# Performance work log

Hardware: AMD Instinct MI355X
Metric: run time of the kernel (lower is better)

The kernel has to match this reference:

```python
import jax, jax.numpy as jnp
import numpy as np

L = 5   # local window size (l)
R = 2   # upsample factor (r)


def setup_inputs() -> dict:
    key = jax.random.key(0)
    k0, k1, k2 = jax.random.split(key, 3)
    B, C, H, W, OUT = 4, 128, 64, 64, 128
    x = jax.random.normal(k0, (B, C, H, W), jnp.float32)
    # conv1: in_channels -> l^2, 3x3, pad 1 (with bias, as nn.Conv2d default)
    w1 = jax.random.normal(k1, (L * L, C, 3, 3), jnp.float32) * 0.05
    b1 = jnp.zeros((L * L,), jnp.float32)
    # conv2: 4*in_channels -> out_channels, 1x1 (stored as [out, 4C])
    w2 = jax.random.normal(k2, (OUT, 4 * C), jnp.float32) * 0.05
    b2 = jnp.zeros((OUT,), jnp.float32)
    return {"x": x, "w1": w1, "b1": b1, "w2": w2, "b2": b2}


def _upsample2_nearest(t):
    # nearest-neighbor x2 upsample on NCHW
    return jnp.repeat(jnp.repeat(t, R, axis=2), R, axis=3)


def reference(x, w1, b1, w2, b2):
    B, C, H, W = x.shape
    # conv1 (3x3, SAME) -> [B, L^2, H, W]
    k = jax.lax.conv_general_dilated(
        x, w1, window_strides=(1, 1), padding='SAME',
        dimension_numbers=('NCHW', 'OIHW', 'NCHW')) + b1[None, :, None, None]
    # nearest x2 upsample then softmax over the L^2 channel dim
    k = _upsample2_nearest(k)                 # [B, L^2, 2H, 2W]
    k = jax.nn.softmax(k, axis=1)
    # non-overlapping RxR block extraction (unfold size=R, step=R twice)
    # -> [B, L^2, H, W, R^2], last-dim order (row-offset, col-offset)
    k = k.reshape(B, L * L, H, R, W, R).transpose(0, 1, 2, 4, 3, 5)
    k = k.reshape(B, L * L, H, W, R * R)
    # overlapping LxL window extraction of the input (unfold size=L, step=1)
    pad = L // 2
    xp = jnp.pad(x, ((0, 0), (0, 0), (pad, pad), (pad, pad)))
    wins = jnp.stack(
        [xp[:, :, i:i + H, j:j + W] for i in range(L) for j in range(L)],
        axis=-1)                               # [B, C, H, W, L^2]
    # per-pixel matmul: [C, L^2] @ [L^2, R^2] -> [B, H, W, C, R^2]
    out = jnp.einsum('bchwk,bkhwr->bhwcr', wins, k)
    # flatten (C, R^2) -> 4C (C-major, matching torch reshape), back to NCHW
    out = out.reshape(B, H, W, C * R * R).transpose(0, 3, 1, 2)
    out = _upsample2_nearest(out)              # [B, 4C, 2H, 2W]
    # conv2: 1x1 -> out_channels
    out = jnp.einsum('bchw,oc->bohw', out, w2) + b2[None, :, None, None]
    return out
```

## Files before the change

### kernel.cpp

```cpp
#include <hip/hip_runtime.h>
#include <math.h>

#define BB   4
#define CC   128
#define HH   64
#define WW   64
#define OUTC 128
#define KK   25

typedef __attribute__((ext_vector_type(8))) short short8;
typedef __attribute__((ext_vector_type(4))) float floatx4;

__device__ __forceinline__ unsigned short f32_to_bf16(float v) {
    unsigned int u = __float_as_uint(v);
    u += 0x7fffu + ((u >> 16) & 1u);
    return (unsigned short)(u >> 16);
}
__device__ __forceinline__ float bf16_to_f32(unsigned short h) {
    return __uint_as_float(((unsigned int)h) << 16);
}

__global__ void prep_kernel(const float* __restrict__ w2,
                            const float* __restrict__ w1,
                            unsigned short* __restrict__ w2o,
                            unsigned short* __restrict__ w1f) {
    int i = blockIdx.x * 256 + threadIdx.x;
    if (i < 16384) {
        int o = i >> 7, c = i & 127;
        const float* p = w2 + o * (4 * CC) + c * 4;
        w2o[o * CC + c] = f32_to_bf16(p[0] + p[1] + p[2] + p[3]);
    } else {
        int f = i - 16384;
        int i8 = f & 7;  int rest = f >> 3;
        int lane = rest & 63; rest >>= 6;
        int ks = rest & 3;  rest >>= 2;
        int mt = rest & 1;  rest >>= 1;
        int dydx = rest % 9;
        int wt   = rest / 9;
        int kk = mt * 16 + (lane & 15);
        int c  = ks * 32 + (lane >> 4) * 8 + i8;
        unsigned short o16 = 0;
        if (kk < KK) {
            float v = w1[(size_t)(kk * CC + c) * 9 + dydx];
            unsigned short hi = f32_to_bf16(v);
            o16 = wt ? f32_to_bf16(v - bf16_to_f32(hi)) : hi;
        }
        w1f[f] = o16;
    }
}

__global__ __launch_bounds__(512, 2) void fused_kernel(
        const float* __restrict__ x,
        const unsigned short* __restrict__ w1f,
        const unsigned short* __restrict__ w2o,
        const float* __restrict__ b1,
        const float* __restrict__ b2,
        float* __restrict__ out) {
    __shared__ unsigned short xs_hi[3 * 68 * 128];
    __shared__ unsigned short xs_lo[3 * 68 * 128];
    __shared__ float pk[KK * 64];
    __shared__ float blds[32];
    unsigned short* sKT = xs_hi;

    int bid0 = blockIdx.x;
    int bid  = (bid0 & 7) * 32 + (bid0 >> 3);
    int h = bid & 63;
    int b = bid >> 6;
    int t = threadIdx.x;
    int lane = t & 63;
    int wv = t >> 6;

    const float* xb = x + (size_t)b * CC * (HH * WW);

    if (t < KK) blds[t] = b1[t];
    {
        int j = lane + 2;
        int swz = (j & 15) << 3;
        for (int ci = 0; ci < 16; ++ci) {
            int c  = wv * 16 + ci;
            int cs = c ^ swz;
            const float* xc = xb + (size_t)c * (HH * WW);
            #pragma unroll
            for (int r = 0; r < 3; ++r) {
                int y = h - 1 + r;
                float v = (y >= 0 && y < HH) ? xc[y * WW + lane] : 0.f;
                unsigned short hi = f32_to_bf16(v);
                unsigned short lo = f32_to_bf16(v - bf16_to_f32(hi));
                xs_hi[(r * 68 + j) * 128 + cs] = hi;
                xs_lo[(r * 68 + j) * 128 + cs] = lo;
            }
        }
        for (int i = t; i < 3 * 4 * 128; i += 512) {
            int c = i & 127; int rem = i >> 7;
            int jj = rem & 3; int r = rem >> 2;
            int j2 = (jj < 2) ? jj : 64 + jj;
            int cs2 = c ^ ((j2 & 15) << 3);
            xs_hi[(r * 68 + j2) * 128 + cs2] = 0;
            xs_lo[(r * 68 + j2) * 128 + cs2] = 0;
        }
    }
    __syncthreads();

    int fpx = lane & 15, quad = lane >> 4;
    int mt = wv & 1, ntw = wv >> 1;
    int pxb = ntw * 16 + fpx;
    floatx4 acc = {0.f, 0.f, 0.f, 0.f};
    for (int dydx = 0; dydx < 9; ++dydx) {
        int r   = dydx / 3;
        int dxm = dydx - 3 * r;
        int j   = pxb + dxm + 1;
        int rowbase = (r * 68 + j) * 128;
        int swz = (j & 15) << 3;
        const unsigned short* whb = w1f + (dydx * 2 + mt) * 2048 + lane * 8;
        #pragma unroll
        for (int ks = 0; ks < 4; ++ks) {
            int cb = (ks * 32 + quad * 8) ^ swz;
            short8 Ah = *(const short8*)(whb + ks * 512);
            short8 Al = *(const short8*)(whb + 36864 + ks * 512);
            short8 Bh = *(const short8*)&xs_hi[rowbase + cb];
            short8 Bl = *(const short8*)&xs_lo[rowbase + cb];
            acc = __builtin_amdgcn_mfma_f32_16x16x32_bf16(Ah, Bh, acc, 0, 0, 0);
            acc = __builtin_amdgcn_mfma_f32_16x16x32_bf16(Ah, Bl, acc, 0, 0, 0);
            acc = __builtin_amdgcn_mfma_f32_16x16x32_bf16(Al, Bh, acc, 0, 0, 0);
        }
    }
    #pragma unroll
    for (int reg = 0; reg < 4; ++reg) {
        int kk = mt * 16 + quad * 4 + reg;
        if (kk < KK) pk[kk * 64 + pxb] = acc[reg] + blds[kk];
    }
    __syncthreads();

    int pp2 = t & 31, cw = t >> 5;

    float2 lg[KK];
    #pragma unroll
    for (int k = 0; k < KK; ++k) lg[k] = *(const float2*)&pk[k * 64 + 2 * pp2];
    float m0 = -1e30f, m1 = -1e30f;
    #pragma unroll
    for (int k = 0; k < KK; ++k) { m0 = fmaxf(m0, lg[k].x); m1 = fmaxf(m1, lg[k].y); }
    float s0 = 0.f, s1 = 0.f;
    #pragma unroll
    for (int k = 0; k < KK; ++k) {
        lg[k].x = __expf(lg[k].x - m0); s0 += lg[k].x;
        lg[k].y = __expf(lg[k].y - m1); s1 += lg[k].y;
    }
    float i0 = 1.f / s0, i1 = 1.f / s1;
    #pragma unroll
    for (int k = 0; k < KK; ++k) { lg[k].x *= i0; lg[k].y *= i1; }

    int colg = 2 * pp2 - 2;
    int coff[3]; float cmask[3];
    #pragma unroll
    for (int jx = 0; jx < 3; ++jx) {
        int cg = colg + 2 * jx;
        cmask[jx] = (cg >= 0 && cg <= WW - 2) ? 1.f : 0.f;
        coff[jx]  = min(max(cg, 0), WW - 2);
    }
    int yoff[5]; float msk[15];
    #pragma unroll
    for (int di = 0; di < 5; ++di) {
        int y = h + di - 2;
        float rm = (y >= 0 && y < HH) ? 1.f : 0.f;
        yoff[di] = min(max(y, 0), HH - 1) * WW;
        #pragma unroll
        for (int jx = 0; jx < 3; ++jx) msk[di * 3 + jx] = rm * cmask[jx];
    }

    #pragma unroll 2
    for (int i8 = 0; i8 < 8; ++i8) {
        int c = i8 * 16 + cw;
        const float* xc = xb + (size_t)c * (HH * WW);
        float2 xv[15];
        #pragma unroll
        for (int di = 0; di < 5; ++di)
            #pragma unroll
            for (int jx = 0; jx < 3; ++jx) {
                float2 v = *(const float2*)(xc + yoff[di] + coff[jx]);
                float mm = msk[di * 3 + jx];
                xv[di * 3 + jx] = make_float2(v.x * mm, v.y * mm);
            }
        float t0 = 0.f, t1 = 0.f;
        #pragma unroll
        for (int di = 0; di < 5; ++di) {
            float2 x01 = xv[di * 3 + 0];
            float2 x23 = xv[di * 3 + 1];
            float2 x45 = xv[di * 3 + 2];
            t0 += lg[di*5+0].x * x01.x + lg[di*5+1].x * x01.y
                + lg[di*5+2].x * x23.x + lg[di*5+3].x * x23.y
                + lg[di*5+4].x * x45.x;
            t1 += lg[di*5+0].y * x01.y + lg[di*5+1].y * x23.x
                + lg[di*5+2].y * x23.y + lg[di*5+3].y * x45.x
                + lg[di*5+4].y * x45.y;
        }
        sKT[(2 * pp2) * 136 + c]     = f32_to_bf16(t0);
        sKT[(2 * pp2 + 1) * 136 + c] = f32_to_bf16(t1);
    }
    __syncthreads();

    floatx4 am[4] = {{0.f,0.f,0.f,0.f},{0.f,0.f,0.f,0.f},
                     {0.f,0.f,0.f,0.f},{0.f,0.f,0.f,0.f}};
    #pragma unroll
    for (int ks = 0; ks < 4; ++ks) {
        short8 af = *(const short8*)&w2o[(size_t)(16*wv + fpx) * CC + ks*32 + quad*8];
        #pragma unroll
        for (int nt = 0; nt < 4; ++nt) {
            short8 bf = *(const short8*)&sKT[(16*nt + fpx) * 136 + ks*32 + quad*8];
            am[nt] = __builtin_amdgcn_mfma_f32_16x16x32_bf16(af, bf, am[nt], 0, 0, 0);
        }
    }

    float* ob = out + (size_t)b * OUTC * (4 * HH * WW);
    int y0 = 2 * h;
    #pragma unroll
    for (int nt = 0; nt < 4; ++nt) {
        #pragma unroll
        for (int reg = 0; reg < 4; ++reg) {
            int o   = 16*wv + quad*4 + reg;
            int pxo = 16*nt + fpx;
            float v = am[nt][reg] + b2[o];
            float2 v2 = make_float2(v, v);
            float* r0p = ob + ((size_t)o * (2*HH) + y0) * (2*WW) + 2*pxo;
            *(float2*)(r0p)        = v2;
            *(float2*)(r0p + 2*WW) = v2;
        }
    }
}

extern "C" void kernel_launch(void* const* d_in, const int* in_sizes, int n_in,
                              void* d_out, int out_size, void* d_ws, size_t ws_size,
                              hipStream_t stream) {
    const float* x  = (const float*)d_in[0];
    const float* w1 = (const float*)d_in[1];
    const float* b1 = (const float*)d_in[2];
    const float* w2 = (const float*)d_in[3];
    const float* b2 = (const float*)d_in[4];
    float* out = (float*)d_out;

    unsigned short* w2o = (unsigned short*)d_ws;
    unsigned short* w1f = w2o + (size_t)OUTC * CC;

    prep_kernel<<<(16384 + 73728) / 256, 256, 0, stream>>>(w2, w1, w2o, w1f);
    fused_kernel<<<BB * HH, 512, 0, stream>>>(x, w1f, w2o, b1, b2, out);
}
```

Before: 102.1 us.

## Split each row into four 16-pixel column tiles with 128-thread blocks

Each block now handles a 16-pixel column slice of one row instead of the full 64-pixel row, giving 1024 blocks of 128 threads instead of 256 blocks of 512. Shared-memory staging shrinks to a 20-column halo window, and the halo columns are now loaded from neighbouring pixels rather than zero-filled. The conv2 MFMA loop is reorganised so that each wave covers 64 output channels across the 16 pixels. The aim is better occupancy and load balance across the CUs. The cost is redundant halo loads and conv1 weight reads repeated in every block, plus a smaller amount of work per wave.

```diff
diff --git a/kernel.cpp b/kernel.cpp
--- a/kernel.cpp
+++ b/kernel.cpp
@@ -7,6 +7,8 @@
 #define WW   64
 #define OUTC 128
 #define KK   25
+#define PXB  16
+#define SJ   20
 
 typedef __attribute__((ext_vector_type(8))) short short8;
 typedef __attribute__((ext_vector_type(4))) float floatx4;
@@ -49,24 +51,25 @@
     }
 }
 
-__global__ __launch_bounds__(512, 2) void fused_kernel(
+__global__ __launch_bounds__(128, 2) void fused_kernel(
         const float* __restrict__ x,
         const unsigned short* __restrict__ w1f,
         const unsigned short* __restrict__ w2o,
         const float* __restrict__ b1,
         const float* __restrict__ b2,
         float* __restrict__ out) {
-    __shared__ unsigned short xs_hi[3 * 68 * 128];
-    __shared__ unsigned short xs_lo[3 * 68 * 128];
-    __shared__ float pk[KK * 64];
+    __shared__ unsigned short xs_hi[3 * SJ * 128];
+    __shared__ unsigned short xs_lo[3 * SJ * 128];
+    __shared__ float pk[KK * PXB];
     __shared__ float blds[32];
     unsigned short* sKT = xs_hi;
 
     int bid0 = blockIdx.x;
-    int bid  = (bid0 & 7) * 32 + (bid0 >> 3);
-    int h = bid & 63;
-    int b = bid >> 6;
-    int t = threadIdx.x;
+    int bid  = (bid0 & 7) * 128 + (bid0 >> 3);
+    int wq = bid & 3;
+    int h  = (bid >> 2) & 63;
+    int b  = bid >> 8;
+    int t  = threadIdx.x;
     int lane = t & 63;
     int wv = t >> 6;
 
@@ -74,42 +77,49 @@
 
     if (t < KK) blds[t] = b1[t];
     {
-        int j = lane + 2;
+        int jj = lane & 15, cc = lane >> 4;
+        int j  = jj + 2;
         int swz = (j & 15) << 3;
         for (int ci = 0; ci < 16; ++ci) {
-            int c  = wv * 16 + ci;
+            int c  = wv * 64 + ci * 4 + cc;
             int cs = c ^ swz;
-            const float* xc = xb + (size_t)c * (HH * WW);
+            const float* xc = xb + (size_t)c * (HH * WW) + wq * 16 + jj;
             #pragma unroll
             for (int r = 0; r < 3; ++r) {
                 int y = h - 1 + r;
-                float v = (y >= 0 && y < HH) ? xc[y * WW + lane] : 0.f;
+                float v = (y >= 0 && y < HH) ? xc[y * WW] : 0.f;
                 unsigned short hi = f32_to_bf16(v);
                 unsigned short lo = f32_to_bf16(v - bf16_to_f32(hi));
-                xs_hi[(r * 68 + j) * 128 + cs] = hi;
-                xs_lo[(r * 68 + j) * 128 + cs] = lo;
+                xs_hi[(r * SJ + j) * 128 + cs] = hi;
+                xs_lo[(r * SJ + j) * 128 + cs] = lo;
             }
         }
-        for (int i = t; i < 3 * 4 * 128; i += 512) {
-            int c = i & 127; int rem = i >> 7;
-            int jj = rem & 3; int r = rem >> 2;
-            int j2 = (jj < 2) ? jj : 64 + jj;
+        for (int i = t; i < 3 * 4 * 128; i += 128) {
+            int jh = i & 3;
+            int c  = (i >> 2) & 127;
+            int r  = i >> 9;
+            int j2 = (jh < 2) ? jh : 16 + jh;
+            int xcol = wq * 16 + j2 - 2;
+            int y = h - 1 + r;
+            float v = (xcol >= 0 && xcol < WW && y >= 0 && y < HH)
+                    ? xb[(size_t)c * (HH * WW) + y * WW + xcol] : 0.f;
+            unsigned short hi = f32_to_bf16(v);
+            unsigned short lo = f32_to_bf16(v - bf16_to_f32(hi));
             int cs2 = c ^ ((j2 & 15) << 3);
-            xs_hi[(r * 68 + j2) * 128 + cs2] = 0;
-            xs_lo[(r * 68 + j2) * 128 + cs2] = 0;
+            xs_hi[(r * SJ + j2) * 128 + cs2] = hi;
+            xs_lo[(r * SJ + j2) * 128 + cs2] = lo;
         }
     }
     __syncthreads();
 
     int fpx = lane & 15, quad = lane >> 4;
-    int mt = wv & 1, ntw = wv >> 1;
-    int pxb = ntw * 16 + fpx;
+    int mt = wv;
     floatx4 acc = {0.f, 0.f, 0.f, 0.f};
     for (int dydx = 0; dydx < 9; ++dydx) {
         int r   = dydx / 3;
         int dxm = dydx - 3 * r;
-        int j   = pxb + dxm + 1;
-        int rowbase = (r * 68 + j) * 128;
+        int j   = fpx + dxm + 1;
+        int rowbase = (r * SJ + j) * 128;
         int swz = (j & 15) << 3;
         const unsigned short* whb = w1f + (dydx * 2 + mt) * 2048 + lane * 8;
         #pragma unroll
@@ -127,15 +137,15 @@
     #pragma unroll
     for (int reg = 0; reg < 4; ++reg) {
         int kk = mt * 16 + quad * 4 + reg;
-        if (kk < KK) pk[kk * 64 + pxb] = acc[reg] + blds[kk];
+        if (kk < KK) pk[kk * PXB + fpx] = acc[reg] + blds[kk];
     }
     __syncthreads();
 
-    int pp2 = t & 31, cw = t >> 5;
+    int pp2 = t & 7, cw = t >> 3;
 
     float2 lg[KK];
     #pragma unroll
-    for (int k = 0; k < KK; ++k) lg[k] = *(const float2*)&pk[k * 64 + 2 * pp2];
+    for (int k = 0; k < KK; ++k) lg[k] = *(const float2*)&pk[k * PXB + 2 * pp2];
     float m0 = -1e30f, m1 = -1e30f;
     #pragma unroll
     for (int k = 0; k < KK; ++k) { m0 = fmaxf(m0, lg[k].x); m1 = fmaxf(m1, lg[k].y); }
@@ -149,7 +159,7 @@
     #pragma unroll
     for (int k = 0; k < KK; ++k) { lg[k].x *= i0; lg[k].y *= i1; }
 
-    int colg = 2 * pp2 - 2;
+    int colg = wq * 16 + 2 * pp2 - 2;
     int coff[3]; float cmask[3];
     #pragma unroll
     for (int jx = 0; jx < 3; ++jx) {
@@ -202,23 +212,24 @@
                      {0.f,0.f,0.f,0.f},{0.f,0.f,0.f,0.f}};
     #pragma unroll
     for (int ks = 0; ks < 4; ++ks) {
-        short8 af = *(const short8*)&w2o[(size_t)(16*wv + fpx) * CC + ks*32 + quad*8];
-        #pragma unroll
-        for (int nt = 0; nt < 4; ++nt) {
-            short8 bf = *(const short8*)&sKT[(16*nt + fpx) * 136 + ks*32 + quad*8];
-            am[nt] = __builtin_amdgcn_mfma_f32_16x16x32_bf16(af, bf, am[nt], 0, 0, 0);
+        short8 bf = *(const short8*)&sKT[fpx * 136 + ks*32 + quad*8];
+        #pragma unroll
+        for (int mt2 = 0; mt2 < 4; ++mt2) {
+            short8 af = *(const short8*)&w2o[(size_t)(64*wv + 16*mt2 + fpx) * CC
+                                             + ks*32 + quad*8];
+            am[mt2] = __builtin_amdgcn_mfma_f32_16x16x32_bf16(af, bf, am[mt2], 0, 0, 0);
         }
     }
 
     float* ob = out + (size_t)b * OUTC * (4 * HH * WW);
     int y0 = 2 * h;
-    #pragma unroll
-    for (int nt = 0; nt < 4; ++nt) {
+    int pxo = wq * 16 + fpx;
+    #pragma unroll
+    for (int mt2 = 0; mt2 < 4; ++mt2) {
         #pragma unroll
         for (int reg = 0; reg < 4; ++reg) {
-            int o   = 16*wv + quad*4 + reg;
-            int pxo = 16*nt + fpx;
-            float v = am[nt][reg] + b2[o];
+            int o = 64*wv + 16*mt2 + quad*4 + reg;
+            float v = am[mt2][reg] + b2[o];
             float2 v2 = make_float2(v, v);
             float* r0p = ob + ((size_t)o * (2*HH) + y0) * (2*WW) + 2*pxo;
             *(float2*)(r0p)        = v2;
@@ -241,5 +252,5 @@
     unsigned short* w1f = w2o + (size_t)OUTC * CC;
 
     prep_kernel<<<(16384 + 73728) / 256, 256, 0, stream>>>(w2, w1, w2o, w1f);
-    fused_kernel<<<BB * HH, 512, 0, stream>>>(x, w1f, w2o, b1, b2, out);
-}
+    fused_kernel<<<BB * HH * 4, 128, 0, stream>>>(x, w1f, w2o, b1, b2, out);
+}
```

Result: slower. 104.8 us (+2.7%).
